# Kernel tuning notes

Measured on AMD Instinct MI355X. Metric: run time of the kernel, lower is better.

Reference implementation:

```python
import jax, jax.numpy as jnp
import numpy as np

B, S, D, H, DFF, L, V = 256, 77, 512, 8, 2048, 12, 49408
HD = D // H
EPS = 1e-5


def setup_inputs() -> dict:
    key = jax.random.key(0)
    ks = jax.random.split(key, 12)
    s = 0.02
    n = lambda k, shape: s * jax.random.normal(k, shape, dtype=jnp.float32)
    return {
        "input_ids": jax.random.randint(ks[0], (B, S), 0, V),
        "attention_mask": jnp.ones((B, S), dtype=jnp.int32),
        "tok_emb": n(ks[1], (V, D)),
        "pos_emb": n(ks[2], (S, D)),
        "ln1_w": jnp.ones((L, D)), "ln1_b": jnp.zeros((L, D)),
        "q_w": n(ks[3], (L, D, D)), "q_b": jnp.zeros((L, D)),
        "k_w": n(ks[4], (L, D, D)), "k_b": jnp.zeros((L, D)),
        "v_w": n(ks[5], (L, D, D)), "v_b": jnp.zeros((L, D)),
        "o_w": n(ks[6], (L, D, D)), "o_b": jnp.zeros((L, D)),
        "ln2_w": jnp.ones((L, D)), "ln2_b": jnp.zeros((L, D)),
        "fc1_w": n(ks[7], (L, DFF, D)), "fc1_b": jnp.zeros((L, DFF)),
        "fc2_w": n(ks[8], (L, D, DFF)), "fc2_b": jnp.zeros((L, D)),
        "lnf_w": jnp.ones((D,)), "lnf_b": jnp.zeros((D,)),
    }


def layer_norm(x, w, b):
    mu = jnp.mean(x, axis=-1, keepdims=True)
    var = jnp.mean(jnp.square(x - mu), axis=-1, keepdims=True)
    return (x - mu) * jax.lax.rsqrt(var + EPS) * w + b


def quick_gelu(x):
    return x * jax.nn.sigmoid(1.702 * x)


def _encoder(x, mask, layer_params):
    scale = HD ** -0.5

    def heads(t):  # [B,S,D] -> [B,H,S,HD]
        return t.reshape(B, S, H, HD).transpose(0, 2, 1, 3)

    def layer(x, p):
        (ln1w, ln1b, qw, qb, kw, kb, vw, vb, ow, ob,
         ln2w, ln2b, f1w, f1b, f2w, f2b) = p
        h = layer_norm(x, ln1w, ln1b)
        q = heads((h @ qw.T + qb) * scale)
        k = heads(h @ kw.T + kb)
        v = heads(h @ vw.T + vb)
        scores = jnp.einsum('bhqd,bhkd->bhqk', q, k) + mask
        probs = jax.nn.softmax(scores, axis=-1)
        a = jnp.einsum('bhqk,bhkd->bhqd', probs, v)
        a = a.transpose(0, 2, 1, 3).reshape(B, S, D) @ ow.T + ob
        x = x + a
        h = layer_norm(x, ln2w, ln2b)
        h = quick_gelu(h @ f1w.T + f1b)
        h = h @ f2w.T + f2b
        return x + h, None

    x, _ = jax.lax.scan(layer, x, layer_params)
    return x


def reference(input_ids, attention_mask, tok_emb, pos_emb,
              ln1_w, ln1_b, q_w, q_b, k_w, k_b, v_w, v_b, o_w, o_b,
              ln2_w, ln2_b, fc1_w, fc1_b, fc2_w, fc2_b, lnf_w, lnf_b):
    x = tok_emb[input_ids] + pos_emb[None]
    neg = jnp.finfo(x.dtype).min
    causal = jnp.triu(jnp.full((S, S), neg, x.dtype), k=1)[None, None]  # [1,1,S,S]
    pad = (1.0 - attention_mask.astype(x.dtype))[:, None, None, :] * neg  # [B,1,1,S]
    mask = causal + pad  # [B,1,S,S]
    layer_params = (ln1_w, ln1_b, q_w, q_b, k_w, k_b, v_w, v_b, o_w, o_b,
                    ln2_w, ln2_b, fc1_w, fc1_b, fc2_w, fc2_b)
    x = _encoder(x, mask, layer_params)
    last_hidden = layer_norm(x, lnf_w, lnf_b)
    # pooled output: eot token = argmax of input_ids (CLIP convention)
    pooled = last_hidden[jnp.arange(B), jnp.argmax(input_ids, axis=-1)]
    return last_hidden, pooled
```

## Files before the change

### kernel.cpp

```cpp
#include <hip/hip_runtime.h>
#include <math.h>

constexpr int BATCH  = 256;
constexpr int SEQ    = 77;
constexpr int DMODEL = 512;
constexpr int NHEAD  = 8;
constexpr int DHEAD  = 64;
constexpr int DFF    = 2048;
constexpr int NLAYER = 12;
constexpr int NTOK   = BATCH * SEQ;
constexpr int NQKV   = 3 * DMODEL;
constexpr float NEGBIG = -3.402823466e38f;

typedef __attribute__((ext_vector_type(8))) short bf16x8;
typedef __attribute__((ext_vector_type(4))) float f32x4;
typedef __attribute__((ext_vector_type(8))) unsigned short u16x8;

typedef __attribute__((address_space(3))) unsigned char lds_u8;
typedef const __attribute__((address_space(1))) unsigned char g_u8;

__device__ __forceinline__ unsigned short f2bf(float f) {
    unsigned u = __float_as_uint(f);
    u = (u + 0x7FFF + ((u >> 16) & 1)) >> 16;
    return (unsigned short)u;
}

#define VMCNT4 asm volatile("s_waitcnt vmcnt(4)" ::: "memory")
#define LGKM0  asm volatile("s_waitcnt lgkmcnt(0)" ::: "memory")
#define SCHEDB __builtin_amdgcn_sched_barrier(0)
#define BARRIER do { SCHEDB; __builtin_amdgcn_s_barrier(); SCHEDB; } while (0)

__global__ __launch_bounds__(256) void conv_qkv_kernel(
    const float* __restrict__ qw, const float* __restrict__ kw,
    const float* __restrict__ vw, unsigned short* __restrict__ dst)
{
    int i4 = blockIdx.x * 256 + threadIdx.x;
    int e = i4 * 4;
    int l = e / (NQKV * DMODEL);
    int rem = e - l * (NQKV * DMODEL);
    int row = rem >> 9;
    int k   = rem & 511;
    const float* src;
    float scale = 1.0f;
    size_t lbase = (size_t)l * DMODEL * DMODEL;
    if (row < 512)       { src = qw + lbase + (size_t)row * DMODEL + k; scale = 0.125f; }
    else if (row < 1024) { src = kw + lbase + (size_t)(row - 512) * DMODEL + k; }
    else                 { src = vw + lbase + (size_t)(row - 1024) * DMODEL + k; }
    float4 v = *(const float4*)src;
    ushort4 o;
    o.x = f2bf(v.x * scale); o.y = f2bf(v.y * scale);
    o.z = f2bf(v.z * scale); o.w = f2bf(v.w * scale);
    *(ushort4*)&dst[e] = o;
}

__global__ __launch_bounds__(256) void conv_kernel(
    const float* __restrict__ src, unsigned short* __restrict__ dst)
{
    int e = (blockIdx.x * 256 + threadIdx.x) * 4;
    float4 v = *(const float4*)&src[e];
    ushort4 o;
    o.x = f2bf(v.x); o.y = f2bf(v.y); o.z = f2bf(v.z); o.w = f2bf(v.w);
    *(ushort4*)&dst[e] = o;
}

__global__ __launch_bounds__(256) void bias_qkv_kernel(
    const float* __restrict__ qb, const float* __restrict__ kb,
    const float* __restrict__ vb, float* __restrict__ dst)
{
    int e = blockIdx.x * 256 + threadIdx.x;
    int l = e / NQKV;
    int row = e - l * NQKV;
    float v;
    if (row < 512)       v = qb[l * DMODEL + row] * 0.125f;
    else if (row < 1024) v = kb[l * DMODEL + row - 512];
    else                 v = vb[l * DMODEL + row - 1024];
    dst[e] = v;
}

__global__ __launch_bounds__(256) void embed_kernel(
    const int* __restrict__ ids, const float* __restrict__ tok,
    const float* __restrict__ pos, float* __restrict__ x)
{
    int f = blockIdx.x * 256 + threadIdx.x;
    int total = NTOK * (DMODEL / 4);
    if (f >= total) return;
    int n  = f >> 7;
    int d4 = f & 127;
    int s  = n % SEQ;
    int id = ids[n];
    float4 t = *(const float4*)&tok[(size_t)id * DMODEL + d4 * 4];
    float4 p = *(const float4*)&pos[(size_t)s  * DMODEL + d4 * 4];
    float4 o; o.x = t.x + p.x; o.y = t.y + p.y; o.z = t.z + p.z; o.w = t.w + p.w;
    *(float4*)&x[(size_t)n * DMODEL + d4 * 4] = o;
}

template <bool BF16OUT>
__global__ __launch_bounds__(256) void ln_kernel(
    const float* __restrict__ x, const float* __restrict__ w,
    const float* __restrict__ b, void* __restrict__ out, int nrows)
{
    int row = blockIdx.x * 4 + (threadIdx.x >> 6);
    if (row >= nrows) return;
    int ln = threadIdx.x & 63;
    const float* xr = x + (size_t)row * DMODEL + ln * 8;
    float4 v0 = *(const float4*)xr;
    float4 v1 = *(const float4*)(xr + 4);
    float va[8] = {v0.x, v0.y, v0.z, v0.w, v1.x, v1.y, v1.z, v1.w};
    float sum = 0.f, sq = 0.f;
#pragma unroll
    for (int j = 0; j < 8; ++j) { sum += va[j]; sq = fmaf(va[j], va[j], sq); }
#pragma unroll
    for (int o = 32; o; o >>= 1) { sum += __shfl_xor(sum, o); sq += __shfl_xor(sq, o); }
    float mu  = sum * (1.0f / DMODEL);
    float var = sq * (1.0f / DMODEL) - mu * mu;
    var = fmaxf(var, 0.0f);
    float inv = 1.0f / sqrtf(var + 1e-5f);
    const float* wp = w + ln * 8;
    const float* bp = b + ln * 8;
    float o8[8];
#pragma unroll
    for (int j = 0; j < 8; ++j) o8[j] = (va[j] - mu) * inv * wp[j] + bp[j];
    if (BF16OUT) {
        u16x8 pk;
#pragma unroll
        for (int j = 0; j < 8; ++j) pk[j] = f2bf(o8[j]);
        *(u16x8*)((unsigned short*)out + (size_t)row * DMODEL + ln * 8) = pk;
    } else {
        float* op = (float*)out + (size_t)row * DMODEL + ln * 8;
        *(float4*)op       = make_float4(o8[0], o8[1], o8[2], o8[3]);
        *(float4*)(op + 4) = make_float4(o8[4], o8[5], o8[6], o8[7]);
    }
}

template <int MODE, bool OUTBF>
__global__ __launch_bounds__(512, 2) void gemm8_bf16(
    const unsigned short* __restrict__ A, const unsigned short* __restrict__ W,
    const float* __restrict__ bias, const float* __restrict__ R,
    void* __restrict__ Cout, int M, int N, int K, int gx)
{
    __shared__ __align__(16) char lds[131072];
    const int nwg = gridDim.x;
    const int wg  = blockIdx.x;
    const int q8  = nwg >> 3, r8 = nwg & 7;
    const int xcd = wg & 7, pos = wg >> 3;
    const int start = (xcd < r8) ? xcd * (q8 + 1) : r8 * (q8 + 1) + (xcd - r8) * q8;
    const int newid = start + pos;
    const int by = newid / gx;
    const int bx = newid - by * gx;
    const int m0 = by * 256;
    const int n0 = bx * 256;

    const int tid  = threadIdx.x;
    const int wid  = tid >> 6;
    const int lane = tid & 63;
    const int wr   = wid >> 2;
    const int wc   = wid & 3;
    const int lhi  = lane >> 4;
    const int llo  = lane & 15;

    const int srow  = tid >> 3;
    const int cglob = (tid & 7) ^ (srow & 7);
    const unsigned short* Ap = A + (size_t)(m0 + srow) * K + cglob * 8;
    const unsigned short* Wp = W + (size_t)(n0 + srow) * K + cglob * 8;
    const int NT  = K >> 6;
    const int NT2 = K >> 7;

    const int cb0 = ((0 * 4 + lhi) ^ (llo & 7)) * 16;
    const int cb1 = ((1 * 4 + lhi) ^ (llo & 7)) * 16;
    const int rbA0 = (wr * 128 + 0 * 64 + llo) * 128;
    const int rbA1 = (wr * 128 + 1 * 64 + llo) * 128;
    const int rbB0 = (wc * 64 + 0 * 32 + llo) * 128;
    const int rbB1 = (wc * 64 + 1 * 32 + llo) * 128;

    f32x4 acc[8][4];
#pragma unroll
    for (int i = 0; i < 8; ++i)
#pragma unroll
        for (int j = 0; j < 4; ++j) acc[i][j] = (f32x4){0.f, 0.f, 0.f, 0.f};

    bf16x8 am[4][2], bn0[2][2], bn1[2][2];

    auto stA = [&](int b, int h, int kt) {
#pragma unroll
        for (int i = h * 2; i < h * 2 + 2; ++i)
            __builtin_amdgcn_global_load_lds(
                (g_u8*)(Ap + (size_t)i * 64 * K + kt * 64),
                (lds_u8*)(lds + b * 32768 + i * 8192 + wid * 1024), 16, 0, 0);
    };
    auto stB = [&](int b, int h, int kt) {
#pragma unroll
        for (int i = h * 2; i < h * 2 + 2; ++i)
            __builtin_amdgcn_global_load_lds(
                (g_u8*)(Wp + (size_t)i * 64 * K + kt * 64),
                (lds_u8*)(lds + 65536 + b * 32768 + i * 8192 + wid * 1024), 16, 0, 0);
    };
    auto rdA = [&](int b, int mh) {
        int base = b * 32768 + (mh ? rbA1 : rbA0);
#pragma unroll
        for (int fm = 0; fm < 4; ++fm) {
            am[fm][0] = *(const bf16x8*)(lds + base + fm * 2048 + cb0);
            am[fm][1] = *(const bf16x8*)(lds + base + fm * 2048 + cb1);
        }
    };
    auto rdB = [&](int b, int nh, bf16x8 (&bn)[2][2]) {
        int base = 65536 + b * 32768 + (nh ? rbB1 : rbB0);
#pragma unroll
        for (int fn = 0; fn < 2; ++fn) {
            bn[fn][0] = *(const bf16x8*)(lds + base + fn * 2048 + cb0);
            bn[fn][1] = *(const bf16x8*)(lds + base + fn * 2048 + cb1);
        }
    };
    auto mq = [&](int mh, int nh, bf16x8 (&bn)[2][2]) {
        __builtin_amdgcn_s_setprio(1);
#pragma unroll
        for (int fm = 0; fm < 4; ++fm)
#pragma unroll
            for (int fn = 0; fn < 2; ++fn)
#pragma unroll
                for (int ks = 0; ks < 2; ++ks)
                    acc[mh * 4 + fm][nh * 2 + fn] =
                        __builtin_amdgcn_mfma_f32_16x16x32_bf16(
                            am[fm][ks], bn[fn][ks], acc[mh * 4 + fm][nh * 2 + fn], 0, 0, 0);
        __builtin_amdgcn_s_setprio(0);
    };

    stA(0, 0, 0); stA(0, 1, 0);
    stB(0, 0, 0); stB(0, 1, 0);
    stB(1, 0, 1); stB(1, 1, 1);
    VMCNT4;
    BARRIER;

    for (int it = 0; it < NT2; ++it) {
        const int k1 = 2 * it + 1;
        const int k2 = (2 * it + 2 < NT) ? 2 * it + 2 : NT - 1;
        const int k3 = (2 * it + 3 < NT) ? 2 * it + 3 : NT - 1;
        rdA(0, 0); rdB(0, 0, bn0);
        stA(1, 0, k1);
        LGKM0; BARRIER;
        mq(0, 0, bn0);
        rdB(0, 1, bn1);
        stA(1, 1, k1);
        LGKM0; BARRIER;
        mq(0, 1, bn1);
        rdA(0, 1);
        stB(0, 0, k2);
        LGKM0; BARRIER;
        mq(1, 1, bn1);
        stB(0, 1, k2);
        VMCNT4; BARRIER;
        mq(1, 0, bn0);
        rdA(1, 0); rdB(1, 0, bn0);
        stA(0, 0, k2);
        LGKM0; BARRIER;
        mq(0, 0, bn0);
        rdB(1, 1, bn1);
        stA(0, 1, k2);
        LGKM0; BARRIER;
        mq(0, 1, bn1);
        rdA(1, 1);
        stB(1, 0, k3);
        LGKM0; BARRIER;
        mq(1, 1, bn1);
        stB(1, 1, k3);
        VMCNT4; BARRIER;
        mq(1, 0, bn0);
    }

    if (OUTBF) {
        unsigned short* sb = (unsigned short*)lds;
#pragma unroll
        for (int j = 0; j < 4; ++j) {
            int colL = wc * 64 + j * 16 + llo;
            float bv = bias[n0 + colL];
#pragma unroll
            for (int i = 0; i < 8; ++i) {
                int rowL = wr * 128 + i * 16 + lhi * 4;
#pragma unroll
                for (int r = 0; r < 4; ++r) {
                    float o = acc[i][j][r] + bv;
                    if (MODE == 2) o = o / (1.0f + __expf(-1.702f * o));
                    sb[(rowL + r) * 256 + colL] = f2bf(o);
                }
            }
        }
        __syncthreads();
        const int l5 = lane & 31, lh2 = lane >> 5;
#pragma unroll
        for (int rr = 0; rr < 16; ++rr) {
            int rowL = rr * 16 + wid * 2 + lh2;
            u16x8 v = *(const u16x8*)&sb[rowL * 256 + l5 * 8];
            *(u16x8*)((unsigned short*)Cout + (size_t)(m0 + rowL) * N + n0 + l5 * 8) = v;
        }
    } else {
        float* sf = (float*)lds;
#pragma unroll
        for (int mh = 0; mh < 2; ++mh) {
            if (mh) __syncthreads();
            if (wr == mh) {
#pragma unroll
                for (int j = 0; j < 4; ++j) {
                    int colL = wc * 64 + j * 16 + llo;
                    float bv = bias[n0 + colL];
#pragma unroll
                    for (int i = 0; i < 8; ++i) {
                        int rowL = i * 16 + lhi * 4;
#pragma unroll
                        for (int r = 0; r < 4; ++r)
                            sf[(rowL + r) * 256 + colL] = acc[i][j][r] + bv;
                    }
                }
            }
            __syncthreads();
#pragma unroll
            for (int rr = 0; rr < 16; ++rr) {
                int rowL = rr * 8 + wid;
                size_t gidx = (size_t)(m0 + mh * 128 + rowL) * N + n0 + lane * 4;
                f32x4 v = *(const f32x4*)&sf[rowL * 256 + lane * 4];
                if (MODE == 3) {
                    f32x4 rv = *(const f32x4*)&R[gidx];
                    v = v + rv;
                }
                *(f32x4*)((float*)Cout + gidx) = v;
            }
        }
    }
}

__global__ __launch_bounds__(256) void attn_mfma_kernel(
    const unsigned short* __restrict__ qkv, const int* __restrict__ amask,
    unsigned short* __restrict__ out)
{
    const int bh = blockIdx.x;
    const int b = bh >> 3;
    const int h = bh & 7;
    __shared__ __align__(16) char smem[68160];
    char* Qs = smem;
    char* Ks = smem + 10240;
    char* Vt = smem;
    char* Pb = smem + 20480;
    float* ss = (float*)(smem + 40960);
    float* padm = (float*)(smem + 67840);
    const int tid  = threadIdx.x;
    const int wid  = tid >> 6;
    const int lane = tid & 63;
    const int llo  = lane & 15;
    const int lhi  = lane >> 4;

    const size_t vbase = ((size_t)(b * SEQ)) * NQKV + 1024 + h * DHEAD;
    bf16x8 vr0, vr1, vr2;
    {
        int c0 = tid, c1 = tid + 256, c2 = tid + 512;
        vr0 = *(const bf16x8*)&qkv[vbase + (size_t)(c0 >> 3) * NQKV + (c0 & 7) * 8];
        vr1 = *(const bf16x8*)&qkv[vbase + (size_t)(c1 >> 3) * NQKV + (c1 & 7) * 8];
        if (c2 < 616)
            vr2 = *(const bf16x8*)&qkv[vbase + (size_t)(c2 >> 3) * NQKV + (c2 & 7) * 8];
    }

    if (tid < 160) {
        int r = tid >> 1, ch = 10 + (tid & 1);
        bf16x8 z;
#pragma unroll
        for (int j = 0; j < 8; ++j) z[j] = 0;
        *(bf16x8*)(Pb + r * 256 + ((ch ^ (r & 7)) * 16)) = z;
    }

    for (int f = tid; f < 640; f += 256) {
        int r = f >> 3, c = f & 7;
        bf16x8 pq, pk;
        if (r < SEQ) {
            size_t g = ((size_t)(b * SEQ + r)) * NQKV + h * DHEAD + c * 8;
            pq = *(const bf16x8*)&qkv[g];
            pk = *(const bf16x8*)&qkv[g + 512];
        } else {
#pragma unroll
            for (int j = 0; j < 8; ++j) { pq[j] = 0; pk[j] = 0; }
        }
        int byte = r * 128 + ((c * 16) ^ ((r & 7) << 4));
        *(bf16x8*)(Qs + byte) = pq;
        *(bf16x8*)(Ks + byte) = pk;
    }
    for (int s = tid; s < SEQ; s += 256)
        padm[s] = (1.0f - (float)amask[b * SEQ + s]) * NEGBIG;
    __syncthreads();

    for (int t = wid; t < 25; t += 4) {
        int rt = t / 5, ct = t % 5;
        int ar = rt * 16 + llo;
        int br = ct * 16 + llo;
        int aswz = (ar & 7) << 4;
        int bswz = (br & 7) << 4;
        bf16x8 a0 = *(const bf16x8*)(Qs + ar * 128 + ((lhi * 16) ^ aswz));
        bf16x8 a1 = *(const bf16x8*)(Qs + ar * 128 + (((lhi + 4) * 16) ^ aswz));
        bf16x8 b0 = *(const bf16x8*)(Ks + br * 128 + ((lhi * 16) ^ bswz));
        bf16x8 b1 = *(const bf16x8*)(Ks + br * 128 + (((lhi + 4) * 16) ^ bswz));
        f32x4 acc = (f32x4){0.f, 0.f, 0.f, 0.f};
        acc = __builtin_amdgcn_mfma_f32_16x16x32_bf16(a0, b0, acc, 0, 0, 0);
        acc = __builtin_amdgcn_mfma_f32_16x16x32_bf16(a1, b1, acc, 0, 0, 0);
        int ki = ct * 16 + llo;
#pragma unroll
        for (int r = 0; r < 4; ++r) {
            int qi = rt * 16 + lhi * 4 + r;
            ss[qi * 84 + ki] = (ki > qi || ki >= SEQ) ? NEGBIG : (acc[r] + padm[ki]);
        }
    }
    __syncthreads();

    {
        auto writeV = [&](int c, bf16x8 v) {
            int s = c >> 3, d8 = (c & 7) * 8;
            int chunk16 = (s >> 3) * 16, within = (s & 7) * 2;
#pragma unroll
            for (int j = 0; j < 8; ++j) {
                int d = d8 + j;
                *(short*)(Vt + d * 256 + (chunk16 ^ ((d & 7) << 4)) + within) = v[j];
            }
        };
        writeV(tid, vr0);
        writeV(tid + 256, vr1);
        if (tid + 512 < 616) writeV(tid + 512, vr2);
    }

    {
        const int g = lane >> 4;
        const int c = lane & 15;
#pragma unroll
        for (int pass = 0; pass < 5; ++pass) {
            int r = pass * 16 + wid * 4 + g;
            float v0 = ss[r * 84 + c];
            float v1 = ss[r * 84 + c + 16];
            float v2 = ss[r * 84 + c + 32];
            float v3 = ss[r * 84 + c + 48];
            float v4 = ss[r * 84 + c + 64];
            float m = fmaxf(fmaxf(fmaxf(v0, v1), fmaxf(v2, v3)), v4);
#pragma unroll
            for (int o = 8; o; o >>= 1) m = fmaxf(m, __shfl_xor(m, o));
            float e0 = __expf(v0 - m), e1 = __expf(v1 - m), e2 = __expf(v2 - m);
            float e3 = __expf(v3 - m), e4 = __expf(v4 - m);
            float tsum = e0 + e1 + e2 + e3 + e4;
#pragma unroll
            for (int o = 8; o; o >>= 1) tsum += __shfl_xor(tsum, o);
            float rinv = 1.0f / tsum;
            int rswz = (r & 7) << 4;
            int rb = r * 256;
            float ev[5] = {e0, e1, e2, e3, e4};
#pragma unroll
            for (int i = 0; i < 5; ++i) {
                int col = c + i * 16;
                *(short*)(Pb + rb + (((col >> 3) * 16) ^ rswz) + (col & 7) * 2) =
                    (short)f2bf(ev[i] * rinv);
            }
        }
    }
    __syncthreads();

    for (int t = wid; t < 20; t += 4) {
        int rt = t >> 2, ct = t & 3;
        int ar = rt * 16 + llo;
        int br = ct * 16 + llo;
        int aswz = (ar & 7) << 4;
        int bswz = (br & 7) << 4;
        f32x4 acc = (f32x4){0.f, 0.f, 0.f, 0.f};
#pragma unroll
        for (int kc = 0; kc < 3; ++kc) {
            bf16x8 af  = *(const bf16x8*)(Pb + ar * 256 + (((kc * 4 + lhi) * 16) ^ aswz));
            bf16x8 bf_ = *(const bf16x8*)(Vt + br * 256 + (((kc * 4 + lhi) * 16) ^ bswz));
            acc = __builtin_amdgcn_mfma_f32_16x16x32_bf16(af, bf_, acc, 0, 0, 0);
        }
        int d = ct * 16 + llo;
#pragma unroll
        for (int r = 0; r < 4; ++r) {
            int qi = rt * 16 + lhi * 4 + r;
            if (qi < SEQ)
                out[((size_t)(b * SEQ + qi)) * DMODEL + h * DHEAD + d] = f2bf(acc[r]);
        }
    }
}

__global__ __launch_bounds__(64) void pool_kernel(
    const int* __restrict__ ids, const float* __restrict__ lh,
    float* __restrict__ pooled)
{
    int b = blockIdx.x;
    int ln = threadIdx.x;
    __shared__ int sidx;
    if (ln == 0) {
        int best = ids[b * SEQ]; int bi = 0;
        for (int s = 1; s < SEQ; ++s) {
            int vv = ids[b * SEQ + s];
            if (vv > best) { best = vv; bi = s; }
        }
        sidx = bi;
    }
    __syncthreads();
    const float* src = lh + ((size_t)(b * SEQ + sidx)) * DMODEL + ln * 8;
    float* dst = pooled + (size_t)b * DMODEL + ln * 8;
    float4 a = *(const float4*)src;
    float4 c = *(const float4*)(src + 4);
    *(float4*)dst       = a;
    *(float4*)(dst + 4) = c;
}

extern "C" void kernel_launch(void* const* d_in, const int* in_sizes, int n_in,
                              void* d_out, int out_size, void* d_ws, size_t ws_size,
                              hipStream_t stream) {
    const int*   ids   = (const int*)d_in[0];
    const int*   amask = (const int*)d_in[1];
    const float* tok   = (const float*)d_in[2];
    const float* pos   = (const float*)d_in[3];
    const float* ln1w  = (const float*)d_in[4];
    const float* ln1b  = (const float*)d_in[5];
    const float* qw    = (const float*)d_in[6];
    const float* qbias = (const float*)d_in[7];
    const float* kw    = (const float*)d_in[8];
    const float* kbias = (const float*)d_in[9];
    const float* vw    = (const float*)d_in[10];
    const float* vbias = (const float*)d_in[11];
    const float* ow    = (const float*)d_in[12];
    const float* obias = (const float*)d_in[13];
    const float* ln2w  = (const float*)d_in[14];
    const float* ln2b  = (const float*)d_in[15];
    const float* f1w   = (const float*)d_in[16];
    const float* f1b   = (const float*)d_in[17];
    const float* f2w   = (const float*)d_in[18];
    const float* f2b   = (const float*)d_in[19];
    const float* lnfw  = (const float*)d_in[20];
    const float* lnfb  = (const float*)d_in[21];

    char* p = (char*)d_ws;
    float* x = (float*)p;                      p += (size_t)NTOK * DMODEL * 4;
    unsigned short* hbuf = (unsigned short*)p; p += (size_t)NTOK * DMODEL * 2;
    unsigned short* qkvb = (unsigned short*)p; p += (size_t)NTOK * NQKV * 2;
    unsigned short* ao = (unsigned short*)p;   p += (size_t)NTOK * DMODEL * 2;
    unsigned short* ff = (unsigned short*)p;   p += (size_t)NTOK * DFF * 2;
    unsigned short* wqkv = (unsigned short*)p; p += (size_t)NLAYER * NQKV * DMODEL * 2;
    unsigned short* wo   = (unsigned short*)p; p += (size_t)NLAYER * DMODEL * DMODEL * 2;
    unsigned short* wf1  = (unsigned short*)p; p += (size_t)NLAYER * DFF * DMODEL * 2;
    unsigned short* wf2  = (unsigned short*)p; p += (size_t)NLAYER * DMODEL * DFF * 2;
    float* bqkv = (float*)p;                   p += (size_t)NLAYER * NQKV * 4;

    conv_qkv_kernel<<<(NLAYER * NQKV * DMODEL / 4) / 256, 256, 0, stream>>>(qw, kw, vw, wqkv);
    conv_kernel<<<(NLAYER * DMODEL * DMODEL / 4) / 256, 256, 0, stream>>>(ow, wo);
    conv_kernel<<<(NLAYER * DFF * DMODEL / 4) / 256, 256, 0, stream>>>(f1w, wf1);
    conv_kernel<<<(NLAYER * DMODEL * DFF / 4) / 256, 256, 0, stream>>>(f2w, wf2);
    bias_qkv_kernel<<<(NLAYER * NQKV) / 256, 256, 0, stream>>>(qbias, kbias, vbias, bqkv);

    embed_kernel<<<(NTOK * (DMODEL / 4) + 255) / 256, 256, 0, stream>>>(ids, tok, pos, x);

    const int MB = NTOK / 256;
    dim3 gqkv(MB * (NQKV / 256));
    dim3 g512(MB * (DMODEL / 256));
    dim3 g2048(MB * (DFF / 256));

    for (int l = 0; l < NLAYER; ++l) {
        const size_t wD2 = (size_t)l * DMODEL * DMODEL;
        const size_t wDF = (size_t)l * DFF * DMODEL;
        const size_t oD  = (size_t)l * DMODEL;
        const size_t oF  = (size_t)l * DFF;

        ln_kernel<true><<<NTOK / 4, 256, 0, stream>>>(x, ln1w + oD, ln1b + oD, hbuf, NTOK);
        gemm8_bf16<0, true><<<gqkv, 512, 0, stream>>>(
            hbuf, wqkv + (size_t)l * NQKV * DMODEL, bqkv + (size_t)l * NQKV, nullptr,
            qkvb, NTOK, NQKV, DMODEL, NQKV / 256);
        attn_mfma_kernel<<<BATCH * NHEAD, 256, 0, stream>>>(qkvb, amask, ao);
        gemm8_bf16<3, false><<<g512, 512, 0, stream>>>(
            ao, wo + wD2, obias + oD, x, x, NTOK, DMODEL, DMODEL, DMODEL / 256);
        ln_kernel<true><<<NTOK / 4, 256, 0, stream>>>(x, ln2w + oD, ln2b + oD, hbuf, NTOK);
        gemm8_bf16<2, true><<<g2048, 512, 0, stream>>>(
            hbuf, wf1 + wDF, f1b + oF, nullptr, ff, NTOK, DFF, DMODEL, DFF / 256);
        gemm8_bf16<3, false><<<g512, 512, 0, stream>>>(
            ff, wf2 + wDF, f2b + oD, x, x, NTOK, DMODEL, DFF, DMODEL / 256);
    }

    float* outf = (float*)d_out;
    ln_kernel<false><<<NTOK / 4, 256, 0, stream>>>(x, lnfw, lnfb, outf, NTOK);
    pool_kernel<<<BATCH, 64, 0, stream>>>(ids, outf, outf + (size_t)NTOK * DMODEL);
}
```

Measured before the change: 3.319 ms.

## Add 128-row GEMM variant for N=512 projections and pad epilogue LDS rows

Adds a gemm8h_bf16 kernel that uses 128x256 output tiles, and uses it for the attention output projection and FC2 (N=512). Those GEMMs previously launched only 154 workgroups with 256x256 tiles. Halving the M tile doubles the workgroup count so more CUs are busy, at the cost of less weight reuse per tile. Separately, the epilogue LDS staging rows are padded (stride 264/260) in both kernels to reduce bank conflicts, which slightly enlarges the original kernel's shared memory.

New measurement: 3.473 ms. 4.6% more time.

```diff
diff --git a/kernel.cpp b/kernel.cpp
--- a/kernel.cpp
+++ b/kernel.cpp
@@ -138,7 +138,7 @@
     const float* __restrict__ bias, const float* __restrict__ R,
     void* __restrict__ Cout, int M, int N, int K, int gx)
 {
-    __shared__ __align__(16) char lds[131072];
+    __shared__ __align__(16) char lds[135168];
     const int nwg = gridDim.x;
     const int wg  = blockIdx.x;
     const int q8  = nwg >> 3, r8 = nwg & 7;
@@ -279,7 +279,7 @@
                 for (int r = 0; r < 4; ++r) {
                     float o = acc[i][j][r] + bv;
                     if (MODE == 2) o = o / (1.0f + __expf(-1.702f * o));
-                    sb[(rowL + r) * 256 + colL] = f2bf(o);
+                    sb[(rowL + r) * 264 + colL] = f2bf(o);
                 }
             }
         }
@@ -288,7 +288,7 @@
 #pragma unroll
         for (int rr = 0; rr < 16; ++rr) {
             int rowL = rr * 16 + wid * 2 + lh2;
-            u16x8 v = *(const u16x8*)&sb[rowL * 256 + l5 * 8];
+            u16x8 v = *(const u16x8*)&sb[rowL * 264 + l5 * 8];
             *(u16x8*)((unsigned short*)Cout + (size_t)(m0 + rowL) * N + n0 + l5 * 8) = v;
         }
     } else {
@@ -306,7 +306,7 @@
                         int rowL = i * 16 + lhi * 4;
 #pragma unroll
                         for (int r = 0; r < 4; ++r)
-                            sf[(rowL + r) * 256 + colL] = acc[i][j][r] + bv;
+                            sf[(rowL + r) * 260 + colL] = acc[i][j][r] + bv;
                     }
                 }
             }
@@ -315,7 +315,195 @@
             for (int rr = 0; rr < 16; ++rr) {
                 int rowL = rr * 8 + wid;
                 size_t gidx = (size_t)(m0 + mh * 128 + rowL) * N + n0 + lane * 4;
-                f32x4 v = *(const f32x4*)&sf[rowL * 256 + lane * 4];
+                f32x4 v = *(const f32x4*)&sf[rowL * 260 + lane * 4];
+                if (MODE == 3) {
+                    f32x4 rv = *(const f32x4*)&R[gidx];
+                    v = v + rv;
+                }
+                *(f32x4*)((float*)Cout + gidx) = v;
+            }
+        }
+    }
+}
+
+template <int MODE, bool OUTBF>
+__global__ __launch_bounds__(512, 2) void gemm8h_bf16(
+    const unsigned short* __restrict__ A, const unsigned short* __restrict__ W,
+    const float* __restrict__ bias, const float* __restrict__ R,
+    void* __restrict__ Cout, int M, int N, int K, int gx)
+{
+    __shared__ __align__(16) char lds[98304];
+    const int nwg = gridDim.x;
+    const int wg  = blockIdx.x;
+    const int q8  = nwg >> 3, r8 = nwg & 7;
+    const int xcd = wg & 7, pos = wg >> 3;
+    const int start = (xcd < r8) ? xcd * (q8 + 1) : r8 * (q8 + 1) + (xcd - r8) * q8;
+    const int newid = start + pos;
+    const int by = newid / gx;
+    const int bx = newid - by * gx;
+    const int m0 = by * 128;
+    const int n0 = bx * 256;
+
+    const int tid  = threadIdx.x;
+    const int wid  = tid >> 6;
+    const int lane = tid & 63;
+    const int wr   = wid >> 2;
+    const int wc   = wid & 3;
+    const int lhi  = lane >> 4;
+    const int llo  = lane & 15;
+
+    const int srow  = tid >> 3;
+    const int cglob = (tid & 7) ^ (srow & 7);
+    const unsigned short* Ap = A + (size_t)(m0 + srow) * K + cglob * 8;
+    const unsigned short* Wp = W + (size_t)(n0 + srow) * K + cglob * 8;
+    const int NT  = K >> 6;
+    const int NT2 = K >> 7;
+
+    const int cb0 = ((0 * 4 + lhi) ^ (llo & 7)) * 16;
+    const int cb1 = ((1 * 4 + lhi) ^ (llo & 7)) * 16;
+
+    f32x4 acc[4][4];
+#pragma unroll
+    for (int i = 0; i < 4; ++i)
+#pragma unroll
+        for (int j = 0; j < 4; ++j) acc[i][j] = (f32x4){0.f, 0.f, 0.f, 0.f};
+
+    bf16x8 am[2][2], bn0[2][2], bn1[2][2];
+
+    auto stA = [&](int b, int h, int kt) {
+        __builtin_amdgcn_global_load_lds(
+            (g_u8*)(Ap + (size_t)h * 64 * K + kt * 64),
+            (lds_u8*)(lds + b * 16384 + h * 8192 + wid * 1024), 16, 0, 0);
+    };
+    auto stB = [&](int b, int h, int kt) {
+#pragma unroll
+        for (int i = h * 2; i < h * 2 + 2; ++i)
+            __builtin_amdgcn_global_load_lds(
+                (g_u8*)(Wp + (size_t)i * 64 * K + kt * 64),
+                (lds_u8*)(lds + 32768 + b * 32768 + i * 8192 + wid * 1024), 16, 0, 0);
+    };
+    auto rdA = [&](int b, int mh) {
+        int base = b * 16384 + (wr * 64 + mh * 32 + llo) * 128;
+#pragma unroll
+        for (int fm = 0; fm < 2; ++fm) {
+            am[fm][0] = *(const bf16x8*)(lds + base + fm * 2048 + cb0);
+            am[fm][1] = *(const bf16x8*)(lds + base + fm * 2048 + cb1);
+        }
+    };
+    auto rdB = [&](int b, int nh, bf16x8 (&bn)[2][2]) {
+        int base = 32768 + b * 32768 + (wc * 64 + nh * 32 + llo) * 128;
+#pragma unroll
+        for (int fn = 0; fn < 2; ++fn) {
+            bn[fn][0] = *(const bf16x8*)(lds + base + fn * 2048 + cb0);
+            bn[fn][1] = *(const bf16x8*)(lds + base + fn * 2048 + cb1);
+        }
+    };
+    auto mq = [&](int mh, int nh, bf16x8 (&bn)[2][2]) {
+        __builtin_amdgcn_s_setprio(1);
+#pragma unroll
+        for (int fm = 0; fm < 2; ++fm)
+#pragma unroll
+            for (int fn = 0; fn < 2; ++fn)
+#pragma unroll
+                for (int ks = 0; ks < 2; ++ks)
+                    acc[mh * 2 + fm][nh * 2 + fn] =
+                        __builtin_amdgcn_mfma_f32_16x16x32_bf16(
+                            am[fm][ks], bn[fn][ks], acc[mh * 2 + fm][nh * 2 + fn], 0, 0, 0);
+        __builtin_amdgcn_s_setprio(0);
+    };
+
+    stA(0, 0, 0); stA(0, 1, 0);
+    stB(0, 0, 0); stB(0, 1, 0);
+    stB(1, 0, 1); stB(1, 1, 1);
+    VMCNT4;
+    BARRIER;
+
+    for (int it = 0; it < NT2; ++it) {
+        const int k1 = 2 * it + 1;
+        const int k2 = (2 * it + 2 < NT) ? 2 * it + 2 : NT - 1;
+        const int k3 = (2 * it + 3 < NT) ? 2 * it + 3 : NT - 1;
+        rdA(0, 0); rdB(0, 0, bn0);
+        stA(1, 0, k1);
+        LGKM0; BARRIER;
+        mq(0, 0, bn0);
+        rdB(0, 1, bn1);
+        stA(1, 1, k1);
+        LGKM0; BARRIER;
+        mq(0, 1, bn1);
+        rdA(0, 1);
+        stB(0, 0, k2);
+        LGKM0; BARRIER;
+        mq(1, 1, bn1);
+        stB(0, 1, k2);
+        VMCNT4; BARRIER;
+        mq(1, 0, bn0);
+        rdA(1, 0); rdB(1, 0, bn0);
+        stA(0, 0, k2);
+        LGKM0; BARRIER;
+        mq(0, 0, bn0);
+        rdB(1, 1, bn1);
+        stA(0, 1, k2);
+        LGKM0; BARRIER;
+        mq(0, 1, bn1);
+        rdA(1, 1);
+        stB(1, 0, k3);
+        LGKM0; BARRIER;
+        mq(1, 1, bn1);
+        stB(1, 1, k3);
+        VMCNT4; BARRIER;
+        mq(1, 0, bn0);
+    }
+
+    if (OUTBF) {
+        unsigned short* sb = (unsigned short*)lds;
+#pragma unroll
+        for (int j = 0; j < 4; ++j) {
+            int colL = wc * 64 + j * 16 + llo;
+            float bv = bias[n0 + colL];
+#pragma unroll
+            for (int i = 0; i < 4; ++i) {
+                int rowL = wr * 64 + i * 16 + lhi * 4;
+#pragma unroll
+                for (int r = 0; r < 4; ++r) {
+                    float o = acc[i][j][r] + bv;
+                    if (MODE == 2) o = o / (1.0f + __expf(-1.702f * o));
+                    sb[(rowL + r) * 264 + colL] = f2bf(o);
+                }
+            }
+        }
+        __syncthreads();
+        const int l5 = lane & 31, lh2 = lane >> 5;
+#pragma unroll
+        for (int rr = 0; rr < 8; ++rr) {
+            int rowL = rr * 16 + wid * 2 + lh2;
+            u16x8 v = *(const u16x8*)&sb[rowL * 264 + l5 * 8];
+            *(u16x8*)((unsigned short*)Cout + (size_t)(m0 + rowL) * N + n0 + l5 * 8) = v;
+        }
+    } else {
+        float* sf = (float*)lds;
+#pragma unroll
+        for (int mh = 0; mh < 2; ++mh) {
+            if (mh) __syncthreads();
+            if (wr == mh) {
+#pragma unroll
+                for (int j = 0; j < 4; ++j) {
+                    int colL = wc * 64 + j * 16 + llo;
+                    float bv = bias[n0 + colL];
+#pragma unroll
+                    for (int i = 0; i < 4; ++i) {
+                        int rowL = i * 16 + lhi * 4;
+#pragma unroll
+                        for (int r = 0; r < 4; ++r)
+                            sf[(rowL + r) * 260 + colL] = acc[i][j][r] + bv;
+                    }
+                }
+            }
+            __syncthreads();
+#pragma unroll
+            for (int rr = 0; rr < 8; ++rr) {
+                int rowL = rr * 8 + wid;
+                size_t gidx = (size_t)(m0 + mh * 64 + rowL) * N + n0 + lane * 4;
+                f32x4 v = *(const f32x4*)&sf[rowL * 260 + lane * 4];
                 if (MODE == 3) {
                     f32x4 rv = *(const f32x4*)&R[gidx];
                     v = v + rv;
@@ -548,7 +736,7 @@
 
     const int MB = NTOK / 256;
     dim3 gqkv(MB * (NQKV / 256));
-    dim3 g512(MB * (DMODEL / 256));
+    dim3 g512h(2 * (NTOK / 128));
     dim3 g2048(MB * (DFF / 256));
 
     for (int l = 0; l < NLAYER; ++l) {
@@ -562,12 +750,12 @@
             hbuf, wqkv + (size_t)l * NQKV * DMODEL, bqkv + (size_t)l * NQKV, nullptr,
             qkvb, NTOK, NQKV, DMODEL, NQKV / 256);
         attn_mfma_kernel<<<BATCH * NHEAD, 256, 0, stream>>>(qkvb, amask, ao);
-        gemm8_bf16<3, false><<<g512, 512, 0, stream>>>(
+        gemm8h_bf16<3, false><<<g512h, 512, 0, stream>>>(
             ao, wo + wD2, obias + oD, x, x, NTOK, DMODEL, DMODEL, DMODEL / 256);
         ln_kernel<true><<<NTOK / 4, 256, 0, stream>>>(x, ln2w + oD, ln2b + oD, hbuf, NTOK);
         gemm8_bf16<2, true><<<g2048, 512, 0, stream>>>(
             hbuf, wf1 + wDF, f1b + oF, nullptr, ff, NTOK, DFF, DMODEL, DFF / 256);
-        gemm8_bf16<3, false><<<g512, 512, 0, stream>>>(
+        gemm8h_bf16<3, false><<<g512h, 512, 0, stream>>>(
             ff, wf2 + wDF, f2b + oD, x, x, NTOK, DMODEL, DFF, DMODEL / 256);
     }
 
```
